# Performance work log

Measured on AMD Instinct MI355X. Metric: run time of the kernel, lower is better.

Reference implementation:

```python
import jax, jax.numpy as jnp
import numpy as np

B, S, NX = 2, 2048, 1024
N_STATE, N_HEAD = 1024, 16
HEAD_DIM = N_STATE // N_HEAD


def setup_inputs() -> dict:
    key = jax.random.key(0)
    k1, k2, k3 = jax.random.split(key, 3)
    x = jax.random.normal(k1, (B, S, NX), dtype=jnp.float32)
    w_c = jax.random.normal(k2, (NX, 3 * N_STATE), dtype=jnp.float32) * 0.02
    b_c = jnp.zeros((3 * N_STATE,), dtype=jnp.float32)
    w_p = jax.random.normal(k3, (NX, N_STATE), dtype=jnp.float32) * 0.02
    b_p = jnp.zeros((N_STATE,), dtype=jnp.float32)
    return {"x": x, "w_c": w_c, "b_c": b_c, "w_p": w_p, "b_p": b_p}


def reference(x, w_c, b_c, w_p, b_p):
    # c_attn: 1x1 conv == dense over last dim -> [B, S, 3*n_state]
    c = jnp.einsum('bsn,nf->bsf', x, w_c) + b_c
    q, k, v = jnp.split(c, 3, axis=2)

    def split_heads(t):  # [B,S,n_state] -> [B,H,S,D]
        return t.reshape(B, S, N_HEAD, HEAD_DIM).transpose(0, 2, 1, 3)

    q = split_heads(q)
    k = split_heads(k)  # we contract over D directly instead of transposing to [B,H,D,S]
    v = split_heads(v)

    # scores [B,H,S,S], scaled by rsqrt(head_dim) (scale=True)
    w = jnp.einsum('bhqd,bhkd->bhqk', q, k) * jax.lax.rsqrt(jnp.float32(HEAD_DIM))
    # band mask exactly as in source: w*b + -1e9*(1-b)
    band = jnp.tril(jnp.ones((S, S), dtype=jnp.float32))[None, None]
    w = w * band + (-1e9) * (1.0 - band)
    w = jax.nn.softmax(w, axis=-1)
    a = jnp.einsum('bhqk,bhkd->bhqd', w, v)

    # merge heads -> [B,S,n_state]
    a = a.transpose(0, 2, 1, 3).reshape(B, S, N_STATE)
    # c_proj
    out = jnp.einsum('bsn,nf->bsf', a, w_p) + b_p
    return out
```

## Files before the change

kernel.cpp:

```cpp
#include <hip/hip_runtime.h>
#include <math.h>

#define BATCH 2
#define SEQ 2048
#define NX 1024
#define NSTATE 1024
#define NHEAD 16
#define HDIM 64
#define QKV_LD (3*NSTATE)

typedef __attribute__((ext_vector_type(4))) float f32x4;
typedef __attribute__((ext_vector_type(8))) short bf16x8;

__device__ __forceinline__ unsigned short f2bf(float x) {
    unsigned int u = __float_as_uint(x);
    u = (u + 0x7FFFu + ((u >> 16) & 1u)) >> 16;
    return (unsigned short)u;
}

__device__ __forceinline__ unsigned int cvtpk_bf16(float a, float b) {
    unsigned int r;
    asm("v_cvt_pk_bf16_f32 %0, %1, %2" : "=v"(r) : "v"(a), "v"(b));
    return r;
}

#define GLL(src, dst) __builtin_amdgcn_global_load_lds( \
    (const __attribute__((address_space(1))) void*)(src), \
    (__attribute__((address_space(3))) void*)(dst), 16, 0, 0)

__global__ __launch_bounds__(256) void prep_kernel(
    const float* __restrict__ x, const float* __restrict__ w_c,
    const float* __restrict__ w_p,
    unsigned short* __restrict__ xbf, unsigned short* __restrict__ wcT,
    unsigned short* __restrict__ wpT)
{
    const int bx = blockIdx.x;
    const int t = threadIdx.x;
    if (bx < 4096) {
        int i = bx * 256 + t;
        float4 v = ((const float4*)x)[i];
        ushort4 o;
        o.x = f2bf(v.x); o.y = f2bf(v.y); o.z = f2bf(v.z); o.w = f2bf(v.w);
        ((ushort4*)xbf)[i] = o;
        return;
    }
    __shared__ float tile[64][65];
    const float* in;
    unsigned short* out;
    int R, C, c0, r0;
    if (bx < 4096 + 768) {
        int idx = bx - 4096;
        in = w_c; out = wcT; R = NX; C = 3 * NSTATE;
        c0 = (idx % 48) * 64; r0 = (idx / 48) * 64;
    } else {
        int idx = bx - 4864;
        in = w_p; out = wpT; R = NX; C = NSTATE;
        c0 = (idx % 16) * 64; r0 = (idx / 16) * 64;
    }
    const int cc = t & 63;
    const int rb = t >> 6;
    #pragma unroll
    for (int i = 0; i < 16; i++) {
        int rr = rb + i * 4;
        tile[rr][cc] = in[(size_t)(r0 + rr) * C + c0 + cc];
    }
    __syncthreads();
    #pragma unroll
    for (int i = 0; i < 16; i++) {
        int rr = rb + i * 4;
        out[(size_t)(c0 + rr) * R + r0 + cc] = f2bf(tile[cc][rr]);
    }
}

__global__ __launch_bounds__(256) void vtrans_kernel(
    const unsigned short* __restrict__ qkv, unsigned short* __restrict__ vt)
{
    __shared__ unsigned short t[64][72];
    const int s0 = blockIdx.x * 64;
    const int bh = blockIdx.y;
    const int b = bh >> 4, h = bh & 15;
    const int r = threadIdx.x >> 2;
    const int cg = (threadIdx.x & 3) * 16;
    const unsigned short* src = qkv + (size_t)(b * SEQ + s0 + r) * QKV_LD
                                + 2 * NSTATE + h * HDIM + cg;
    *(bf16x8*)&t[r][cg]     = *(const bf16x8*)src;
    *(bf16x8*)&t[r][cg + 8] = *(const bf16x8*)(src + 8);
    __syncthreads();
    unsigned short tmp[16];
    #pragma unroll
    for (int i = 0; i < 16; i++) tmp[i] = t[cg + i][r];
    unsigned short* dst = vt + (size_t)(bh * 64 + r) * SEQ + s0 + cg;
    *(bf16x8*)dst       = ((const bf16x8*)tmp)[0];
    *(bf16x8*)(dst + 8) = ((const bf16x8*)tmp)[1];
}

template<bool BF16_OUT>
__global__ __launch_bounds__(256) void gemm_bf16(
    const unsigned short* __restrict__ A,
    const unsigned short* __restrict__ BT,
    const float* __restrict__ bias,
    void* __restrict__ Cv, int M, int N, int K)
{
    __shared__ unsigned short Als[128 * 32];
    __shared__ unsigned short Bls[128 * 32];
    const int tid = threadIdx.x;
    const int wave = tid >> 6, lane = tid & 63;
    const int bm = blockIdx.x * 128, bn = blockIdx.y * 128;
    const int wr = (wave >> 1) * 64, wc = (wave & 1) * 64;

    f32x4 acc[4][4];
    #pragma unroll
    for (int m = 0; m < 4; m++)
        #pragma unroll
        for (int n = 0; n < 4; n++)
            acc[m][n] = (f32x4){0.f, 0.f, 0.f, 0.f};

    const int arow = tid >> 2;
    const int ac8 = (tid & 3) * 8;
    char* alds0 = (char*)Als + wave * 1024;
    char* blds0 = (char*)Bls + wave * 1024;
    const int fr = lane & 15, kq = (lane >> 4) * 8;

    for (int k0 = 0; k0 < K; k0 += 32) {
        const unsigned short* ga0 = A  + (size_t)(bm + arow) * K + k0 + ac8;
        const unsigned short* gb0 = BT + (size_t)(bn + arow) * K + k0 + ac8;
        GLL(ga0, alds0);
        GLL(ga0 + (size_t)64 * K, alds0 + 4096);
        GLL(gb0, blds0);
        GLL(gb0 + (size_t)64 * K, blds0 + 4096);
        __syncthreads();

        bf16x8 af[4], bfr[4];
        #pragma unroll
        for (int m = 0; m < 4; m++)
            af[m] = *(const bf16x8*)&Als[(wr + m * 16 + fr) * 32 + kq];
        #pragma unroll
        for (int n = 0; n < 4; n++)
            bfr[n] = *(const bf16x8*)&Bls[(wc + n * 16 + fr) * 32 + kq];
        #pragma unroll
        for (int m = 0; m < 4; m++)
            #pragma unroll
            for (int n = 0; n < 4; n++)
                acc[m][n] = __builtin_amdgcn_mfma_f32_16x16x32_bf16(
                    af[m], bfr[n], acc[m][n], 0, 0, 0);
        __syncthreads();
    }

    const int cr = (lane >> 4) * 4;
    const int ccol = lane & 15;
    #pragma unroll
    for (int m = 0; m < 4; m++) {
        const int row = bm + wr + m * 16 + cr;
        #pragma unroll
        for (int n = 0; n < 4; n++) {
            const int col = bn + wc + n * 16 + ccol;
            const float bv = bias[col];
            #pragma unroll
            for (int j = 0; j < 4; j++) {
                float v = acc[m][n][j] + bv;
                if (BF16_OUT)
                    ((unsigned short*)Cv)[(size_t)(row + j) * N + col] = f2bf(v);
                else
                    ((float*)Cv)[(size_t)(row + j) * N + col] = v;
            }
        }
    }
}

__global__ __launch_bounds__(256) void attn_mfma(
    const unsigned short* __restrict__ qkv,
    const unsigned short* __restrict__ vt,
    unsigned short* __restrict__ a_out)
{
    const int bx = blockIdx.x;
    const int h = blockIdx.y, b = blockIdx.z;
    const int tid = threadIdx.x;
    const int w = tid >> 6, lane = tid & 63;
    const int c = lane & 15, hh = lane >> 4;

    __shared__ unsigned short Kls[2 * 64 * 64];
    __shared__ unsigned short Vls[2 * 64 * 64];
    __shared__ unsigned short Pls[4][16 * 64];

    const float Cc = 0.18033688f;

    const int o0 = tid * 16;
    const int r0 = o0 >> 7, sc0 = (o0 & 127) ^ ((r0 & 7) << 4);
    const int o1 = 4096 + tid * 16;
    const int r1 = o1 >> 7, sc1 = (o1 & 127) ^ ((r1 & 7) << 4);

    char* kld = (char*)Kls + w * 1024;
    char* vld = (char*)Vls + w * 1024;
    const char* gkbase = (const char*)(qkv + (size_t)b * SEQ * QKV_LD + NSTATE + h * HDIM);
    const char* gvbase = (const char*)(vt + (size_t)(b * NHEAD + h) * HDIM * SEQ);

    #define STAGE(kt_, buf_) do { \
        const char* gk = gkbase + (size_t)(kt_) * 64 * 6144; \
        const char* gv = gvbase + (size_t)(kt_) * 128; \
        char* kd = kld + (buf_) * 8192; \
        char* vd = vld + (buf_) * 8192; \
        GLL(gk + (size_t)r0 * 6144 + sc0, kd); \
        GLL(gk + (size_t)r1 * 6144 + sc1, kd + 4096); \
        GLL(gv + (size_t)r0 * 4096 + sc0, vd); \
        GLL(gv + (size_t)r1 * 4096 + sc1, vd + 4096); \
    } while (0)

    for (int phase = 0; phase < 2; phase++) {
        const int qb = phase ? bx : (31 - bx);

        const size_t qrow = (size_t)(b * SEQ + qb * 64 + w * 16 + c);
        const unsigned short* qp = qkv + qrow * QKV_LD + h * HDIM;
        bf16x8 qf0 = *(const bf16x8*)(qp + hh * 8);
        bf16x8 qf1 = *(const bf16x8*)(qp + 32 + hh * 8);

        f32x4 acc_o[4];
        #pragma unroll
        for (int n = 0; n < 4; n++) acc_o[n] = (f32x4){0.f, 0.f, 0.f, 0.f};
        float m_run = -1e30f, l = 0.f;

        const int nkt = qb + 1;
        STAGE(0, 0);
        __syncthreads();

        for (int kt = 0; kt < nkt; kt++) {
            const int cur = kt & 1;
            if (kt + 1 < nkt) STAGE(kt + 1, cur ^ 1);

            const char* kb = (const char*)Kls + cur * 8192;
            const char* vb = (const char*)Vls + cur * 8192;

            f32x4 sacc[4];
            __builtin_amdgcn_s_setprio(1);
            #pragma unroll
            for (int m = 0; m < 4; m++) {
                const int row = m * 16 + c;
                const int sw = (row & 7) << 4;
                bf16x8 kf0 = *(const bf16x8*)(kb + row * 128 + ((hh * 16) ^ sw));
                bf16x8 kf1 = *(const bf16x8*)(kb + row * 128 + ((64 + hh * 16) ^ sw));
                f32x4 z = (f32x4){0.f, 0.f, 0.f, 0.f};
                z = __builtin_amdgcn_mfma_f32_16x16x32_bf16(kf0, qf0, z, 0, 0, 0);
                sacc[m] = __builtin_amdgcn_mfma_f32_16x16x32_bf16(kf1, qf1, z, 0, 0, 0);
            }
            __builtin_amdgcn_s_setprio(0);

            const bool diag = (kt == qb);
            float s[16];
            #pragma unroll
            for (int m = 0; m < 4; m++)
                #pragma unroll
                for (int j = 0; j < 4; j++) {
                    float sv = sacc[m][j];
                    if (diag) {
                        int klocal = m * 16 + hh * 4 + j;
                        if (klocal > w * 16 + c) sv = -1e30f;
                    }
                    s[m * 4 + j] = sv;
                }
            float x0 = fmaxf(s[0], s[1]),  x1 = fmaxf(s[2], s[3]);
            float x2 = fmaxf(s[4], s[5]),  x3 = fmaxf(s[6], s[7]);
            float x4 = fmaxf(s[8], s[9]),  x5 = fmaxf(s[10], s[11]);
            float x6 = fmaxf(s[12], s[13]), x7 = fmaxf(s[14], s[15]);
            float y0 = fmaxf(x0, x1), y1 = fmaxf(x2, x3);
            float y2 = fmaxf(x4, x5), y3 = fmaxf(x6, x7);
            float pmax = fmaxf(fmaxf(y0, y1), fmaxf(y2, y3));
            pmax = fmaxf(pmax, __shfl_xor(pmax, 16));
            pmax = fmaxf(pmax, __shfl_xor(pmax, 32));

            if (!__all(pmax <= m_run + 64.0f)) {
                const float mnew = fmaxf(m_run, pmax);
                const float alpha = exp2f((m_run - mnew) * Cc);
                m_run = mnew;
                l *= alpha;
                const float a0 = __shfl(alpha, hh * 4 + 0);
                const float a1 = __shfl(alpha, hh * 4 + 1);
                const float a2 = __shfl(alpha, hh * 4 + 2);
                const float a3 = __shfl(alpha, hh * 4 + 3);
                #pragma unroll
                for (int n = 0; n < 4; n++) {
                    acc_o[n][0] *= a0; acc_o[n][1] *= a1;
                    acc_o[n][2] *= a2; acc_o[n][3] *= a3;
                }
            }
            const float mc = m_run * Cc;
            float p[16];
            #pragma unroll
            for (int i = 0; i < 16; i++)
                p[i] = exp2f(fmaf(s[i], Cc, -mc));
            {
                float a0 = p[0] + p[1],  a1 = p[2] + p[3];
                float a2 = p[4] + p[5],  a3 = p[6] + p[7];
                float a4 = p[8] + p[9],  a5 = p[10] + p[11];
                float a6 = p[12] + p[13], a7 = p[14] + p[15];
                float b0 = a0 + a1, b1 = a2 + a3, b2 = a4 + a5, b3 = a6 + a7;
                l += (b0 + b1) + (b2 + b3);
            }

            {
                char* pb = (char*)&Pls[w][0] + c * 128;
                const int swp = (c & 7) << 4;
                #pragma unroll
                for (int m = 0; m < 4; m++) {
                    uint2 u;
                    u.x = cvtpk_bf16(p[m * 4 + 0], p[m * 4 + 1]);
                    u.y = cvtpk_bf16(p[m * 4 + 2], p[m * 4 + 3]);
                    *(uint2*)(pb + ((m * 32 + hh * 8) ^ swp)) = u;
                }
            }

            {
                const char* pb = (const char*)&Pls[w][0] + c * 128;
                const int swp = (c & 7) << 4;
                bf16x8 pf0 = *(const bf16x8*)(pb + ((hh * 16) ^ swp));
                bf16x8 pf1 = *(const bf16x8*)(pb + ((64 + hh * 16) ^ swp));
                __builtin_amdgcn_s_setprio(1);
                #pragma unroll
                for (int n = 0; n < 4; n++) {
                    const int row = n * 16 + c;
                    const int sw = (row & 7) << 4;
                    bf16x8 vf0 = *(const bf16x8*)(vb + row * 128 + ((hh * 16) ^ sw));
                    bf16x8 vf1 = *(const bf16x8*)(vb + row * 128 + ((64 + hh * 16) ^ sw));
                    acc_o[n] = __builtin_amdgcn_mfma_f32_16x16x32_bf16(pf0, vf0, acc_o[n], 0, 0, 0);
                    acc_o[n] = __builtin_amdgcn_mfma_f32_16x16x32_bf16(pf1, vf1, acc_o[n], 0, 0, 0);
                }
                __builtin_amdgcn_s_setprio(0);
            }
            __syncthreads();
        }

        l += __shfl_xor(l, 16);
        l += __shfl_xor(l, 32);
        const float linv = 1.f / l;
        const float li0 = __shfl(linv, hh * 4 + 0);
        const float li1 = __shfl(linv, hh * 4 + 1);
        const float li2 = __shfl(linv, hh * 4 + 2);
        const float li3 = __shfl(linv, hh * 4 + 3);
        const size_t orow0 = (size_t)(b * SEQ + qb * 64 + w * 16 + hh * 4);
        #pragma unroll
        for (int n = 0; n < 4; n++) {
            const int col = h * HDIM + n * 16 + c;
            a_out[(orow0 + 0) * NSTATE + col] = f2bf(acc_o[n][0] * li0);
            a_out[(orow0 + 1) * NSTATE + col] = f2bf(acc_o[n][1] * li1);
            a_out[(orow0 + 2) * NSTATE + col] = f2bf(acc_o[n][2] * li2);
            a_out[(orow0 + 3) * NSTATE + col] = f2bf(acc_o[n][3] * li3);
        }
    }
    #undef STAGE
}

extern "C" void kernel_launch(void* const* d_in, const int* in_sizes, int n_in,
                              void* d_out, int out_size, void* d_ws, size_t ws_size,
                              hipStream_t stream)
{
    const float* x   = (const float*)d_in[0];
    const float* w_c = (const float*)d_in[1];
    const float* b_c = (const float*)d_in[2];
    const float* w_p = (const float*)d_in[3];
    const float* b_p = (const float*)d_in[4];
    float* out = (float*)d_out;

    const int M = BATCH * SEQ;

    char* ws = (char*)d_ws;
    unsigned short* qkvbf = (unsigned short*)ws;
    unsigned short* vt    = (unsigned short*)(ws + 25165824);
    unsigned short* xbf   = (unsigned short*)(ws + 25165824 + 8388608);
    unsigned short* wcT   = (unsigned short*)(ws + 25165824 + 2*8388608);
    unsigned short* wpT   = (unsigned short*)(ws + 25165824 + 2*8388608 + 6291456);

    prep_kernel<<<5120, 256, 0, stream>>>(x, w_c, w_p, xbf, wcT, wpT);

    gemm_bf16<true><<<dim3(M / 128, 3 * NSTATE / 128), 256, 0, stream>>>(
        xbf, wcT, b_c, qkvbf, M, 3 * NSTATE, NX);

    vtrans_kernel<<<dim3(SEQ / 64, BATCH * NHEAD), 256, 0, stream>>>(qkvbf, vt);

    attn_mfma<<<dim3(16, NHEAD, BATCH), 256, 0, stream>>>(qkvbf, vt, xbf);

    gemm_bf16<false><<<dim3(M / 128, NSTATE / 128), 256, 0, stream>>>(
        xbf, wpT, b_p, out, M, NSTATE, NX);
}
```

Baseline: 204.1 us.

## Split attention blocks into 32-row query chunks and load V directly to registers

The attention kernel now uses 128-thread blocks, each covering a 32-row query chunk, and launches twice as many blocks. The causal mask accounts for the row offset inside the 64-key tile. V fragments are read straight from global memory into registers instead of being staged through LDS, and the K staging is reworked for two waves. The aim is more parallelism and a smaller LDS footprint, at the cost of K/V tiles being reloaded by more blocks and V loads that are not overlapped through LDS.

```diff
diff --git a/kernel.cpp b/kernel.cpp
--- a/kernel.cpp
+++ b/kernel.cpp
@@ -167,48 +167,43 @@
     }
 }
 
-__global__ __launch_bounds__(256) void attn_mfma(
+__global__ __launch_bounds__(128) void attn_mfma(
     const unsigned short* __restrict__ qkv,
     const unsigned short* __restrict__ vt,
     unsigned short* __restrict__ a_out)
 {
-    const int bx = blockIdx.x;
+    const int cx = blockIdx.x;
     const int h = blockIdx.y, b = blockIdx.z;
     const int tid = threadIdx.x;
     const int w = tid >> 6, lane = tid & 63;
     const int c = lane & 15, hh = lane >> 4;
 
     __shared__ unsigned short Kls[2 * 64 * 64];
-    __shared__ unsigned short Vls[2 * 64 * 64];
-    __shared__ unsigned short Pls[4][16 * 64];
+    __shared__ unsigned short Pls[2][16 * 64];
 
     const float Cc = 0.18033688f;
 
-    const int o0 = tid * 16;
-    const int r0 = o0 >> 7, sc0 = (o0 & 127) ^ ((r0 & 7) << 4);
-    const int o1 = 4096 + tid * 16;
-    const int r1 = o1 >> 7, sc1 = (o1 & 127) ^ ((r1 & 7) << 4);
-
-    char* kld = (char*)Kls + w * 1024;
-    char* vld = (char*)Vls + w * 1024;
+    const int rr = w * 8 + (lane >> 3);
+    const int sc = ((lane & 7) * 16) ^ (((lane >> 3) & 7) << 4);
+
     const char* gkbase = (const char*)(qkv + (size_t)b * SEQ * QKV_LD + NSTATE + h * HDIM);
-    const char* gvbase = (const char*)(vt + (size_t)(b * NHEAD + h) * HDIM * SEQ);
+    const unsigned short* gv = vt + (size_t)(b * NHEAD + h) * HDIM * SEQ;
 
     #define STAGE(kt_, buf_) do { \
-        const char* gk = gkbase + (size_t)(kt_) * 64 * 6144; \
-        const char* gv = gvbase + (size_t)(kt_) * 128; \
-        char* kd = kld + (buf_) * 8192; \
-        char* vd = vld + (buf_) * 8192; \
-        GLL(gk + (size_t)r0 * 6144 + sc0, kd); \
-        GLL(gk + (size_t)r1 * 6144 + sc1, kd + 4096); \
-        GLL(gv + (size_t)r0 * 4096 + sc0, vd); \
-        GLL(gv + (size_t)r1 * 4096 + sc1, vd + 4096); \
+        const char* gk = gkbase + (size_t)(kt_) * 64 * 6144 + sc; \
+        char* kd = (char*)Kls + (buf_) * 8192 + w * 1024; \
+        GLL(gk + (size_t)(rr +  0) * 6144, kd); \
+        GLL(gk + (size_t)(rr + 16) * 6144, kd + 2048); \
+        GLL(gk + (size_t)(rr + 32) * 6144, kd + 4096); \
+        GLL(gk + (size_t)(rr + 48) * 6144, kd + 6144); \
     } while (0)
 
     for (int phase = 0; phase < 2; phase++) {
-        const int qb = phase ? bx : (31 - bx);
-
-        const size_t qrow = (size_t)(b * SEQ + qb * 64 + w * 16 + c);
+        const int chunk = phase ? cx : (63 - cx);
+        const int rowoff = (chunk & 1) * 32;
+        const int qtile = chunk >> 1;
+
+        const size_t qrow = (size_t)(b * SEQ + chunk * 32 + w * 16 + c);
         const unsigned short* qp = qkv + qrow * QKV_LD + h * HDIM;
         bf16x8 qf0 = *(const bf16x8*)(qp + hh * 8);
         bf16x8 qf1 = *(const bf16x8*)(qp + 32 + hh * 8);
@@ -218,7 +213,7 @@
         for (int n = 0; n < 4; n++) acc_o[n] = (f32x4){0.f, 0.f, 0.f, 0.f};
         float m_run = -1e30f, l = 0.f;
 
-        const int nkt = qb + 1;
+        const int nkt = qtile + 1;
         STAGE(0, 0);
         __syncthreads();
 
@@ -226,8 +221,15 @@
             const int cur = kt & 1;
             if (kt + 1 < nkt) STAGE(kt + 1, cur ^ 1);
 
+            bf16x8 vf[4][2];
+            #pragma unroll
+            for (int n = 0; n < 4; n++)
+                #pragma unroll
+                for (int hf = 0; hf < 2; hf++)
+                    vf[n][hf] = *(const bf16x8*)(gv + (size_t)(n * 16 + c) * SEQ
+                                                 + kt * 64 + hf * 32 + hh * 8);
+
             const char* kb = (const char*)Kls + cur * 8192;
-            const char* vb = (const char*)Vls + cur * 8192;
 
             f32x4 sacc[4];
             __builtin_amdgcn_s_setprio(1);
@@ -243,7 +245,7 @@
             }
             __builtin_amdgcn_s_setprio(0);
 
-            const bool diag = (kt == qb);
+            const bool diag = (kt == qtile);
             float s[16];
             #pragma unroll
             for (int m = 0; m < 4; m++)
@@ -252,7 +254,7 @@
                     float sv = sacc[m][j];
                     if (diag) {
                         int klocal = m * 16 + hh * 4 + j;
-                        if (klocal > w * 16 + c) sv = -1e30f;
+                        if (klocal > rowoff + w * 16 + c) sv = -1e30f;
                     }
                     s[m * 4 + j] = sv;
                 }
@@ -315,12 +317,8 @@
                 __builtin_amdgcn_s_setprio(1);
                 #pragma unroll
                 for (int n = 0; n < 4; n++) {
-                    const int row = n * 16 + c;
-                    const int sw = (row & 7) << 4;
-                    bf16x8 vf0 = *(const bf16x8*)(vb + row * 128 + ((hh * 16) ^ sw));
-                    bf16x8 vf1 = *(const bf16x8*)(vb + row * 128 + ((64 + hh * 16) ^ sw));
-                    acc_o[n] = __builtin_amdgcn_mfma_f32_16x16x32_bf16(pf0, vf0, acc_o[n], 0, 0, 0);
-                    acc_o[n] = __builtin_amdgcn_mfma_f32_16x16x32_bf16(pf1, vf1, acc_o[n], 0, 0, 0);
+                    acc_o[n] = __builtin_amdgcn_mfma_f32_16x16x32_bf16(pf0, vf[n][0], acc_o[n], 0, 0, 0);
+                    acc_o[n] = __builtin_amdgcn_mfma_f32_16x16x32_bf16(pf1, vf[n][1], acc_o[n], 0, 0, 0);
                 }
                 __builtin_amdgcn_s_setprio(0);
             }
@@ -334,7 +332,7 @@
         const float li1 = __shfl(linv, hh * 4 + 1);
         const float li2 = __shfl(linv, hh * 4 + 2);
         const float li3 = __shfl(linv, hh * 4 + 3);
-        const size_t orow0 = (size_t)(b * SEQ + qb * 64 + w * 16 + hh * 4);
+        const size_t orow0 = (size_t)(b * SEQ + chunk * 32 + w * 16 + hh * 4);
         #pragma unroll
         for (int n = 0; n < 4; n++) {
             const int col = h * HDIM + n * 16 + c;
@@ -374,7 +372,7 @@
 
     vtrans_kernel<<<dim3(SEQ / 64, BATCH * NHEAD), 256, 0, stream>>>(qkvbf, vt);
 
-    attn_mfma<<<dim3(16, NHEAD, BATCH), 256, 0, stream>>>(qkvbf, vt, xbf);
+    attn_mfma<<<dim3(32, NHEAD, BATCH), 128, 0, stream>>>(qkvbf, vt, xbf);
 
     gemm_bf16<false><<<dim3(M / 128, NSTATE / 128), 256, 0, stream>>>(
         xbf, wpT, b_p, out, M, NSTATE, NX);
```

Result: slower. 233.6 us (+14.5%).

## Remap GEMM blocks per XCD, split attention into per-qblock blocks, smaller proj tiles

Applied to the files above, without the earlier changes.

The QKV GEMM now uses a flat 1D grid whose block index is remapped so each XCD works on a contiguous rectangle of output tiles, aiming for better L2 reuse. The attention kernel launches one block per query tile instead of pairing a long and a short tile in one block, and orders tiles so that light and heavy ones interleave across the schedule. The output projection switches to a new 64x64-tile GEMM with 1024 blocks to fill more CUs. The smaller tile has lower per-block reuse and single-buffered loads, and unpaired attention blocks give up the built-in load balancing of the paired scheme.

```diff
diff --git a/kernel.cpp b/kernel.cpp
--- a/kernel.cpp
+++ b/kernel.cpp
@@ -94,18 +94,24 @@
     *(bf16x8*)(dst + 8) = ((const bf16x8*)tmp)[1];
 }
 
-template<bool BF16_OUT>
+template<int RX, int RY, int NBX, bool BF16_OUT>
 __global__ __launch_bounds__(256) void gemm_bf16(
     const unsigned short* __restrict__ A,
     const unsigned short* __restrict__ BT,
     const float* __restrict__ bias,
     void* __restrict__ Cv, int M, int N, int K)
 {
+    const int flat = blockIdx.x;
+    const int xcd = flat & 7;
+    const int j = flat >> 3;
+    const int bx = (xcd % (NBX / RX)) * RX + (j % RX);
+    const int by = (xcd / (NBX / RX)) * RY + (j / RX);
+
     __shared__ unsigned short Als[128 * 32];
     __shared__ unsigned short Bls[128 * 32];
     const int tid = threadIdx.x;
     const int wave = tid >> 6, lane = tid & 63;
-    const int bm = blockIdx.x * 128, bn = blockIdx.y * 128;
+    const int bm = bx * 128, bn = by * 128;
     const int wr = (wave >> 1) * 64, wc = (wave & 1) * 64;
 
     f32x4 acc[4][4];
@@ -156,12 +162,87 @@
             const int col = bn + wc + n * 16 + ccol;
             const float bv = bias[col];
             #pragma unroll
-            for (int j = 0; j < 4; j++) {
-                float v = acc[m][n][j] + bv;
+            for (int j2 = 0; j2 < 4; j2++) {
+                float v = acc[m][n][j2] + bv;
                 if (BF16_OUT)
-                    ((unsigned short*)Cv)[(size_t)(row + j) * N + col] = f2bf(v);
+                    ((unsigned short*)Cv)[(size_t)(row + j2) * N + col] = f2bf(v);
                 else
-                    ((float*)Cv)[(size_t)(row + j) * N + col] = v;
+                    ((float*)Cv)[(size_t)(row + j2) * N + col] = v;
+            }
+        }
+    }
+}
+
+template<int RX, int RY, int NBX, bool BF16_OUT>
+__global__ __launch_bounds__(256) void gemm_bf16_s(
+    const unsigned short* __restrict__ A,
+    const unsigned short* __restrict__ BT,
+    const float* __restrict__ bias,
+    void* __restrict__ Cv, int M, int N, int K)
+{
+    const int flat = blockIdx.x;
+    const int xcd = flat & 7;
+    const int j = flat >> 3;
+    const int bx = (xcd % (NBX / RX)) * RX + (j % RX);
+    const int by = (xcd / (NBX / RX)) * RY + (j / RX);
+
+    __shared__ unsigned short Als[64 * 32];
+    __shared__ unsigned short Bls[64 * 32];
+    const int tid = threadIdx.x;
+    const int wave = tid >> 6, lane = tid & 63;
+    const int bm = bx * 64, bn = by * 64;
+    const int wr = (wave >> 1) * 32, wc = (wave & 1) * 32;
+
+    f32x4 acc[2][2];
+    #pragma unroll
+    for (int m = 0; m < 2; m++)
+        #pragma unroll
+        for (int n = 0; n < 2; n++)
+            acc[m][n] = (f32x4){0.f, 0.f, 0.f, 0.f};
+
+    const int arow = tid >> 2;
+    const int ac8 = (tid & 3) * 8;
+    char* alds = (char*)Als + tid * 16;
+    char* blds = (char*)Bls + tid * 16;
+    const int fr = lane & 15, kq = (lane >> 4) * 8;
+
+    for (int k0 = 0; k0 < K; k0 += 32) {
+        GLL(A  + (size_t)(bm + arow) * K + k0 + ac8, alds);
+        GLL(BT + (size_t)(bn + arow) * K + k0 + ac8, blds);
+        __syncthreads();
+
+        bf16x8 af[2], bfr[2];
+        #pragma unroll
+        for (int m = 0; m < 2; m++)
+            af[m] = *(const bf16x8*)&Als[(wr + m * 16 + fr) * 32 + kq];
+        #pragma unroll
+        for (int n = 0; n < 2; n++)
+            bfr[n] = *(const bf16x8*)&Bls[(wc + n * 16 + fr) * 32 + kq];
+        #pragma unroll
+        for (int m = 0; m < 2; m++)
+            #pragma unroll
+            for (int n = 0; n < 2; n++)
+                acc[m][n] = __builtin_amdgcn_mfma_f32_16x16x32_bf16(
+                    af[m], bfr[n], acc[m][n], 0, 0, 0);
+        __syncthreads();
+    }
+
+    const int cr = (lane >> 4) * 4;
+    const int ccol = lane & 15;
+    #pragma unroll
+    for (int m = 0; m < 2; m++) {
+        const int row = bm + wr + m * 16 + cr;
+        #pragma unroll
+        for (int n = 0; n < 2; n++) {
+            const int col = bn + wc + n * 16 + ccol;
+            const float bv = bias[col];
+            #pragma unroll
+            for (int j2 = 0; j2 < 4; j2++) {
+                float v = acc[m][n][j2] + bv;
+                if (BF16_OUT)
+                    ((unsigned short*)Cv)[(size_t)(row + j2) * N + col] = f2bf(v);
+                else
+                    ((float*)Cv)[(size_t)(row + j2) * N + col] = v;
             }
         }
     }
@@ -172,8 +253,12 @@
     const unsigned short* __restrict__ vt,
     unsigned short* __restrict__ a_out)
 {
-    const int bx = blockIdx.x;
-    const int h = blockIdx.y, b = blockIdx.z;
+    const int f = blockIdx.x;
+    const int k_ = f >> 8;
+    const int u = (f >> 5) & 7;
+    const int bh = f & 31;
+    const int qb = (k_ & 1) ? (k_ * 8 + 7 - u) : (k_ * 8 + u);
+    const int b = bh >> 4, h = bh & 15;
     const int tid = threadIdx.x;
     const int w = tid >> 6, lane = tid & 63;
     const int c = lane & 15, hh = lane >> 4;
@@ -205,146 +290,142 @@
         GLL(gv + (size_t)r1 * 4096 + sc1, vd + 4096); \
     } while (0)
 
-    for (int phase = 0; phase < 2; phase++) {
-        const int qb = phase ? bx : (31 - bx);
-
-        const size_t qrow = (size_t)(b * SEQ + qb * 64 + w * 16 + c);
-        const unsigned short* qp = qkv + qrow * QKV_LD + h * HDIM;
-        bf16x8 qf0 = *(const bf16x8*)(qp + hh * 8);
-        bf16x8 qf1 = *(const bf16x8*)(qp + 32 + hh * 8);
-
-        f32x4 acc_o[4];
-        #pragma unroll
-        for (int n = 0; n < 4; n++) acc_o[n] = (f32x4){0.f, 0.f, 0.f, 0.f};
-        float m_run = -1e30f, l = 0.f;
-
-        const int nkt = qb + 1;
-        STAGE(0, 0);
+    const size_t qrow = (size_t)(b * SEQ + qb * 64 + w * 16 + c);
+    const unsigned short* qp = qkv + qrow * QKV_LD + h * HDIM;
+    bf16x8 qf0 = *(const bf16x8*)(qp + hh * 8);
+    bf16x8 qf1 = *(const bf16x8*)(qp + 32 + hh * 8);
+
+    f32x4 acc_o[4];
+    #pragma unroll
+    for (int n = 0; n < 4; n++) acc_o[n] = (f32x4){0.f, 0.f, 0.f, 0.f};
+    float m_run = -1e30f, l = 0.f;
+
+    const int nkt = qb + 1;
+    STAGE(0, 0);
+    __syncthreads();
+
+    for (int kt = 0; kt < nkt; kt++) {
+        const int cur = kt & 1;
+        if (kt + 1 < nkt) STAGE(kt + 1, cur ^ 1);
+
+        const char* kb = (const char*)Kls + cur * 8192;
+        const char* vb = (const char*)Vls + cur * 8192;
+
+        f32x4 sacc[4];
+        __builtin_amdgcn_s_setprio(1);
+        #pragma unroll
+        for (int m = 0; m < 4; m++) {
+            const int row = m * 16 + c;
+            const int sw = (row & 7) << 4;
+            bf16x8 kf0 = *(const bf16x8*)(kb + row * 128 + ((hh * 16) ^ sw));
+            bf16x8 kf1 = *(const bf16x8*)(kb + row * 128 + ((64 + hh * 16) ^ sw));
+            f32x4 z = (f32x4){0.f, 0.f, 0.f, 0.f};
+            z = __builtin_amdgcn_mfma_f32_16x16x32_bf16(kf0, qf0, z, 0, 0, 0);
+            sacc[m] = __builtin_amdgcn_mfma_f32_16x16x32_bf16(kf1, qf1, z, 0, 0, 0);
+        }
+        __builtin_amdgcn_s_setprio(0);
+
+        const bool diag = (kt == qb);
+        float s[16];
+        #pragma unroll
+        for (int m = 0; m < 4; m++)
+            #pragma unroll
+            for (int j = 0; j < 4; j++) {
+                float sv = sacc[m][j];
+                if (diag) {
+                    int klocal = m * 16 + hh * 4 + j;
+                    if (klocal > w * 16 + c) sv = -1e30f;
+                }
+                s[m * 4 + j] = sv;
+            }
+        float x0 = fmaxf(s[0], s[1]),  x1 = fmaxf(s[2], s[3]);
+        float x2 = fmaxf(s[4], s[5]),  x3 = fmaxf(s[6], s[7]);
+        float x4 = fmaxf(s[8], s[9]),  x5 = fmaxf(s[10], s[11]);
+        float x6 = fmaxf(s[12], s[13]), x7 = fmaxf(s[14], s[15]);
+        float y0 = fmaxf(x0, x1), y1 = fmaxf(x2, x3);
+        float y2 = fmaxf(x4, x5), y3 = fmaxf(x6, x7);
+        float pmax = fmaxf(fmaxf(y0, y1), fmaxf(y2, y3));
+        pmax = fmaxf(pmax, __shfl_xor(pmax, 16));
+        pmax = fmaxf(pmax, __shfl_xor(pmax, 32));
+
+        if (!__all(pmax <= m_run + 64.0f)) {
+            const float mnew = fmaxf(m_run, pmax);
+            const float alpha = exp2f((m_run - mnew) * Cc);
+            m_run = mnew;
+            l *= alpha;
+            const float a0 = __shfl(alpha, hh * 4 + 0);
+            const float a1 = __shfl(alpha, hh * 4 + 1);
+            const float a2 = __shfl(alpha, hh * 4 + 2);
+            const float a3 = __shfl(alpha, hh * 4 + 3);
+            #pragma unroll
+            for (int n = 0; n < 4; n++) {
+                acc_o[n][0] *= a0; acc_o[n][1] *= a1;
+                acc_o[n][2] *= a2; acc_o[n][3] *= a3;
+            }
+        }
+        const float mc = m_run * Cc;
+        float p[16];
+        #pragma unroll
+        for (int i = 0; i < 16; i++)
+            p[i] = exp2f(fmaf(s[i], Cc, -mc));
+        {
+            float a0 = p[0] + p[1],  a1 = p[2] + p[3];
+            float a2 = p[4] + p[5],  a3 = p[6] + p[7];
+            float a4 = p[8] + p[9],  a5 = p[10] + p[11];
+            float a6 = p[12] + p[13], a7 = p[14] + p[15];
+            float b0 = a0 + a1, b1 = a2 + a3, b2 = a4 + a5, b3 = a6 + a7;
+            l += (b0 + b1) + (b2 + b3);
+        }
+
+        {
+            char* pb = (char*)&Pls[w][0] + c * 128;
+            const int swp = (c & 7) << 4;
+            #pragma unroll
+            for (int m = 0; m < 4; m++) {
+                uint2 u2;
+                u2.x = cvtpk_bf16(p[m * 4 + 0], p[m * 4 + 1]);
+                u2.y = cvtpk_bf16(p[m * 4 + 2], p[m * 4 + 3]);
+                *(uint2*)(pb + ((m * 32 + hh * 8) ^ swp)) = u2;
+            }
+        }
+
+        {
+            const char* pb = (const char*)&Pls[w][0] + c * 128;
+            const int swp = (c & 7) << 4;
+            bf16x8 pf0 = *(const bf16x8*)(pb + ((hh * 16) ^ swp));
+            bf16x8 pf1 = *(const bf16x8*)(pb + ((64 + hh * 16) ^ swp));
+            __builtin_amdgcn_s_setprio(1);
+            #pragma unroll
+            for (int n = 0; n < 4; n++) {
+                const int row = n * 16 + c;
+                const int sw = (row & 7) << 4;
+                bf16x8 vf0 = *(const bf16x8*)(vb + row * 128 + ((hh * 16) ^ sw));
+                bf16x8 vf1 = *(const bf16x8*)(vb + row * 128 + ((64 + hh * 16) ^ sw));
+                acc_o[n] = __builtin_amdgcn_mfma_f32_16x16x32_bf16(pf0, vf0, acc_o[n], 0, 0, 0);
+                acc_o[n] = __builtin_amdgcn_mfma_f32_16x16x32_bf16(pf1, vf1, acc_o[n], 0, 0, 0);
+            }
+            __builtin_amdgcn_s_setprio(0);
+        }
         __syncthreads();
-
-        for (int kt = 0; kt < nkt; kt++) {
-            const int cur = kt & 1;
-            if (kt + 1 < nkt) STAGE(kt + 1, cur ^ 1);
-
-            const char* kb = (const char*)Kls + cur * 8192;
-            const char* vb = (const char*)Vls + cur * 8192;
-
-            f32x4 sacc[4];
-            __builtin_amdgcn_s_setprio(1);
-            #pragma unroll
-            for (int m = 0; m < 4; m++) {
-                const int row = m * 16 + c;
-                const int sw = (row & 7) << 4;
-                bf16x8 kf0 = *(const bf16x8*)(kb + row * 128 + ((hh * 16) ^ sw));
-                bf16x8 kf1 = *(const bf16x8*)(kb + row * 128 + ((64 + hh * 16) ^ sw));
-                f32x4 z = (f32x4){0.f, 0.f, 0.f, 0.f};
-                z = __builtin_amdgcn_mfma_f32_16x16x32_bf16(kf0, qf0, z, 0, 0, 0);
-                sacc[m] = __builtin_amdgcn_mfma_f32_16x16x32_bf16(kf1, qf1, z, 0, 0, 0);
-            }
-            __builtin_amdgcn_s_setprio(0);
-
-            const bool diag = (kt == qb);
-            float s[16];
-            #pragma unroll
-            for (int m = 0; m < 4; m++)
-                #pragma unroll
-                for (int j = 0; j < 4; j++) {
-                    float sv = sacc[m][j];
-                    if (diag) {
-                        int klocal = m * 16 + hh * 4 + j;
-                        if (klocal > w * 16 + c) sv = -1e30f;
-                    }
-                    s[m * 4 + j] = sv;
-                }
-            float x0 = fmaxf(s[0], s[1]),  x1 = fmaxf(s[2], s[3]);
-            float x2 = fmaxf(s[4], s[5]),  x3 = fmaxf(s[6], s[7]);
-            float x4 = fmaxf(s[8], s[9]),  x5 = fmaxf(s[10], s[11]);
-            float x6 = fmaxf(s[12], s[13]), x7 = fmaxf(s[14], s[15]);
-            float y0 = fmaxf(x0, x1), y1 = fmaxf(x2, x3);
-            float y2 = fmaxf(x4, x5), y3 = fmaxf(x6, x7);
-            float pmax = fmaxf(fmaxf(y0, y1), fmaxf(y2, y3));
-            pmax = fmaxf(pmax, __shfl_xor(pmax, 16));
-            pmax = fmaxf(pmax, __shfl_xor(pmax, 32));
-
-            if (!__all(pmax <= m_run + 64.0f)) {
-                const float mnew = fmaxf(m_run, pmax);
-                const float alpha = exp2f((m_run - mnew) * Cc);
-                m_run = mnew;
-                l *= alpha;
-                const float a0 = __shfl(alpha, hh * 4 + 0);
-                const float a1 = __shfl(alpha, hh * 4 + 1);
-                const float a2 = __shfl(alpha, hh * 4 + 2);
-                const float a3 = __shfl(alpha, hh * 4 + 3);
-                #pragma unroll
-                for (int n = 0; n < 4; n++) {
-                    acc_o[n][0] *= a0; acc_o[n][1] *= a1;
-                    acc_o[n][2] *= a2; acc_o[n][3] *= a3;
-                }
-            }
-            const float mc = m_run * Cc;
-            float p[16];
-            #pragma unroll
-            for (int i = 0; i < 16; i++)
-                p[i] = exp2f(fmaf(s[i], Cc, -mc));
-            {
-                float a0 = p[0] + p[1],  a1 = p[2] + p[3];
-                float a2 = p[4] + p[5],  a3 = p[6] + p[7];
-                float a4 = p[8] + p[9],  a5 = p[10] + p[11];
-                float a6 = p[12] + p[13], a7 = p[14] + p[15];
-                float b0 = a0 + a1, b1 = a2 + a3, b2 = a4 + a5, b3 = a6 + a7;
-                l += (b0 + b1) + (b2 + b3);
-            }
-
-            {
-                char* pb = (char*)&Pls[w][0] + c * 128;
-                const int swp = (c & 7) << 4;
-                #pragma unroll
-                for (int m = 0; m < 4; m++) {
-                    uint2 u;
-                    u.x = cvtpk_bf16(p[m * 4 + 0], p[m * 4 + 1]);
-                    u.y = cvtpk_bf16(p[m * 4 + 2], p[m * 4 + 3]);
-                    *(uint2*)(pb + ((m * 32 + hh * 8) ^ swp)) = u;
-                }
-            }
-
-            {
-                const char* pb = (const char*)&Pls[w][0] + c * 128;
-                const int swp = (c & 7) << 4;
-                bf16x8 pf0 = *(const bf16x8*)(pb + ((hh * 16) ^ swp));
-                bf16x8 pf1 = *(const bf16x8*)(pb + ((64 + hh * 16) ^ swp));
-                __builtin_amdgcn_s_setprio(1);
-                #pragma unroll
-                for (int n = 0; n < 4; n++) {
-                    const int row = n * 16 + c;
-                    const int sw = (row & 7) << 4;
-                    bf16x8 vf0 = *(const bf16x8*)(vb + row * 128 + ((hh * 16) ^ sw));
-                    bf16x8 vf1 = *(const bf16x8*)(vb + row * 128 + ((64 + hh * 16) ^ sw));
-                    acc_o[n] = __builtin_amdgcn_mfma_f32_16x16x32_bf16(pf0, vf0, acc_o[n], 0, 0, 0);
-                    acc_o[n] = __builtin_amdgcn_mfma_f32_16x16x32_bf16(pf1, vf1, acc_o[n], 0, 0, 0);
-                }
-                __builtin_amdgcn_s_setprio(0);
-            }
-            __syncthreads();
-        }
-
-        l += __shfl_xor(l, 16);
-        l += __shfl_xor(l, 32);
-        const float linv = 1.f / l;
-        const float li0 = __shfl(linv, hh * 4 + 0);
-        const float li1 = __shfl(linv, hh * 4 + 1);
-        const float li2 = __shfl(linv, hh * 4 + 2);
-        const float li3 = __shfl(linv, hh * 4 + 3);
-        const size_t orow0 = (size_t)(b * SEQ + qb * 64 + w * 16 + hh * 4);
-        #pragma unroll
-        for (int n = 0; n < 4; n++) {
-            const int col = h * HDIM + n * 16 + c;
-            a_out[(orow0 + 0) * NSTATE + col] = f2bf(acc_o[n][0] * li0);
-            a_out[(orow0 + 1) * NSTATE + col] = f2bf(acc_o[n][1] * li1);
-            a_out[(orow0 + 2) * NSTATE + col] = f2bf(acc_o[n][2] * li2);
-            a_out[(orow0 + 3) * NSTATE + col] = f2bf(acc_o[n][3] * li3);
-        }
     }
     #undef STAGE
+
+    l += __shfl_xor(l, 16);
+    l += __shfl_xor(l, 32);
+    const float linv = 1.f / l;
+    const float li0 = __shfl(linv, hh * 4 + 0);
+    const float li1 = __shfl(linv, hh * 4 + 1);
+    const float li2 = __shfl(linv, hh * 4 + 2);
+    const float li3 = __shfl(linv, hh * 4 + 3);
+    const size_t orow0 = (size_t)(b * SEQ + qb * 64 + w * 16 + hh * 4);
+    #pragma unroll
+    for (int n = 0; n < 4; n++) {
+        const int col = h * HDIM + n * 16 + c;
+        a_out[(orow0 + 0) * NSTATE + col] = f2bf(acc_o[n][0] * li0);
+        a_out[(orow0 + 1) * NSTATE + col] = f2bf(acc_o[n][1] * li1);
+        a_out[(orow0 + 2) * NSTATE + col] = f2bf(acc_o[n][2] * li2);
+        a_out[(orow0 + 3) * NSTATE + col] = f2bf(acc_o[n][3] * li3);
+    }
 }
 
 extern "C" void kernel_launch(void* const* d_in, const int* in_sizes, int n_in,
@@ -369,13 +450,13 @@
 
     prep_kernel<<<5120, 256, 0, stream>>>(x, w_c, w_p, xbf, wcT, wpT);
 
-    gemm_bf16<true><<<dim3(M / 128, 3 * NSTATE / 128), 256, 0, stream>>>(
+    gemm_bf16<8, 12, 32, true><<<768, 256, 0, stream>>>(
         xbf, wcT, b_c, qkvbf, M, 3 * NSTATE, NX);
 
     vtrans_kernel<<<dim3(SEQ / 64, BATCH * NHEAD), 256, 0, stream>>>(qkvbf, vt);
 
-    attn_mfma<<<dim3(16, NHEAD, BATCH), 256, 0, stream>>>(qkvbf, vt, xbf);
-
-    gemm_bf16<false><<<dim3(M / 128, NSTATE / 128), 256, 0, stream>>>(
+    attn_mfma<<<1024, 256, 0, stream>>>(qkvbf, vt, xbf);
+
+    gemm_bf16_s<16, 8, 64, false><<<1024, 256, 0, stream>>>(
         xbf, wpT, b_p, out, M, NSTATE, NX);
 }
```

Result: faster. 196.6 us (-3.7%).
